# Performance work log

Measured on AMD Instinct MI355X. Metric: run time of the kernel, lower is better.

## Reference

```python
import jax, jax.numpy as jnp
import numpy as np

B, T, C, H = 8, 1024, 768, 12
M = 8  # extra rows in feats left as zeros (n = M + B*T)
N = M + B * T


def setup_inputs() -> dict:
    key = jax.random.key(0)
    k1, k2, k3, k4, k5 = jax.random.split(key, 5)
    feats = jax.random.normal(k1, (N, C), dtype=jnp.float32)
    amask = jax.random.randint(k2, (B, T), 0, 2).astype(bool)
    Wqkv = jax.random.normal(k3, (3 * C, C), dtype=jnp.float32) * 0.02
    Wp = jax.random.normal(k4, (C, C), dtype=jnp.float32) * 0.02
    bp = jax.random.normal(k5, (C,), dtype=jnp.float32) * 0.001
    return {"feats": feats, "amask": amask, "Wqkv": Wqkv, "Wp": Wp, "bp": bp}


def reference(feats, amask, Wqkv, Wp, bp):
    b, t = amask.shape
    n, c = feats.shape
    m = n - b * t          # rows of feats not touched by attention (stay zero)
    h = H
    d = c // h
    scale = d ** -0.5
    mf = amask.reshape(-1)                      # [b*t] bool
    x = feats[m:]                               # [b*t, c]

    # MaskedLinear(qkv): gather->GEMM->scatter == dense GEMM zeroed at masked-out rows
    qkv = jnp.where(mf[:, None], x @ Wqkv.T, jnp.zeros((), x.dtype))  # [b*t, 3c]
    qkv = qkv.reshape(b, t, 3, h, d).transpose(2, 0, 3, 1, 4)          # [3,b,h,t,d]
    q, k, v = qkv[0], qkv[1], qkv[2]

    # dense SDPA (no attn mask, matching F.scaled_dot_product_attention default)
    att = jax.nn.softmax(jnp.einsum('bhqd,bhkd->bhqk', q, k) * scale, axis=-1)
    o = jnp.einsum('bhqk,bhkd->bhqd', att, v)                          # [b,h,t,d]
    o = o.transpose(0, 2, 1, 3).reshape(b * t, c)                      # [b*t, c]

    # MaskedLinear(proj) with bias; masked-out rows are zero (not bias)
    o = jnp.where(mf[:, None], o @ Wp.T + bp, jnp.zeros((), o.dtype))

    # scatter back into a zero tensor of feats' shape (first m rows zero)
    return jnp.concatenate([jnp.zeros((m, c), feats.dtype), o], axis=0)
```

## Files before the change

### kernel.cpp

```cpp
#include <hip/hip_runtime.h>
#include <hip/hip_bf16.h>


#define BB 8
#define TT 1024
#define CC 768
#define HH 12
#define DD 64
#define MM 8
#define NTOK (BB*TT)
#define NX (NTOK*CC)
#define NWQ (3*CC*CC)
#define NWP (CC*CC)
#define QSCALE 0.18033688011112042f

typedef short bf16x8 __attribute__((ext_vector_type(8)));
typedef float f32x4  __attribute__((ext_vector_type(4)));
typedef float f32x16 __attribute__((ext_vector_type(16)));

__device__ __forceinline__ void gld16(const void* g, void* l) {
  __builtin_amdgcn_global_load_lds(
      (const __attribute__((address_space(1))) void*)g,
      (__attribute__((address_space(3))) void*)l, 16, 0, 0);
}

__device__ __forceinline__ short bf_rne(float f) {
  unsigned u = __float_as_uint(f);
  return (short)((u + 0x7FFFu + ((u >> 16) & 1u)) >> 16);
}
__device__ __forceinline__ short bf_split(float f, short& lo) {
  unsigned u = __float_as_uint(f);
  unsigned hb = (u + 0x7FFFu + ((u >> 16) & 1u)) >> 16;
  float r = f - __uint_as_float(hb << 16);
  lo = bf_rne(r);
  return (short)hb;
}

__global__ __launch_bounds__(256) void split_inputs(
    const float* __restrict__ x, const float* __restrict__ wq,
    const float* __restrict__ wp,
    short* __restrict__ xh, short* __restrict__ wqh,
    short* __restrict__ wph, short* __restrict__ wpl,
    float* __restrict__ out) {
  const int G0 = NX/4, G1 = G0 + NWQ/4, G2 = G1 + NWP/4;
  int i = blockIdx.x * 256 + threadIdx.x;
  if (i < MM*CC/4) {
    float4 z = {0.f, 0.f, 0.f, 0.f};
    ((float4*)out)[i] = z;
  }
  if (i >= G2) return;
  if (i < G1) {
    const float* src = (i < G0) ? x : wq;
    short* dh = (i < G0) ? xh : wqh;
    int li = (i < G0) ? i : i - G0;
    float4 v = *(const float4*)(src + (size_t)li * 4);
    short4 h;
    h.x = bf_rne(v.x); h.y = bf_rne(v.y); h.z = bf_rne(v.z); h.w = bf_rne(v.w);
    *(short4*)(dh + (size_t)li * 4) = h;
  } else {
    int li = i - G1;
    float4 v = *(const float4*)(wp + (size_t)li * 4);
    short4 h, l;
    h.x = bf_split(v.x, l.x);
    h.y = bf_split(v.y, l.y);
    h.z = bf_split(v.z, l.z);
    h.w = bf_split(v.w, l.w);
    *(short4*)(wph + (size_t)li * 4) = h;
    *(short4*)(wpl + (size_t)li * 4) = l;
  }
}

template<bool TRIPLE>
__device__ __forceinline__ void gemm_core_768(
    const short* __restrict__ ah_g, const short* __restrict__ al_g,
    const short* __restrict__ bh_g, const short* __restrict__ bl_g,
    short* Ah, short* Al, short* Bh, short* Bl,
    int m0, int n0, f32x16 (&acc)[2][2],
    int& wm_o, int& wn_o) {
  const int tid = threadIdx.x;
  const int w = tid >> 6, ln = tid & 63;
  const int wm = (w >> 1) * 64, wn = (w & 1) * 64;
  const int sr = ln >> 2;
  const int sc = (((ln & 3) ^ ((ln >> 3) & 3))) * 8;
  const int l31 = ln & 31, lhi = ln >> 5;
  const int key = (l31 >> 1) & 3;
  const int c0 = 2*w, c1 = 2*w + 1;
  const short* gAh0 = ah_g + (size_t)(m0 + c0*16 + sr)*CC + sc;
  const short* gAh1 = ah_g + (size_t)(m0 + c1*16 + sr)*CC + sc;
  const short* gBh0 = bh_g + (size_t)(n0 + c0*16 + sr)*CC + sc;
  const short* gBh1 = bh_g + (size_t)(n0 + c1*16 + sr)*CC + sc;
  const short* gAl0 = TRIPLE ? al_g + (size_t)(m0 + c0*16 + sr)*CC + sc : nullptr;
  const short* gAl1 = TRIPLE ? al_g + (size_t)(m0 + c1*16 + sr)*CC + sc : nullptr;
  const short* gBl0 = TRIPLE ? bl_g + (size_t)(n0 + c0*16 + sr)*CC + sc : nullptr;
  const short* gBl1 = TRIPLE ? bl_g + (size_t)(n0 + c1*16 + sr)*CC + sc : nullptr;
  #pragma unroll
  for (int i = 0; i < 2; i++)
    #pragma unroll
    for (int j = 0; j < 2; j++)
      #pragma unroll
      for (int r = 0; r < 16; r++) acc[i][j][r] = 0.f;

  for (int it = 0; it < 24; ++it) {
    const int ko = it * 32;
    gld16(gAh0 + ko, &Ah[c0*512]);
    gld16(gAh1 + ko, &Ah[c1*512]);
    gld16(gBh0 + ko, &Bh[c0*512]);
    gld16(gBh1 + ko, &Bh[c1*512]);
    if constexpr (TRIPLE) {
      gld16(gAl0 + ko, &Al[c0*512]);
      gld16(gAl1 + ko, &Al[c1*512]);
      gld16(gBl0 + ko, &Bl[c0*512]);
      gld16(gBl1 + ko, &Bl[c1*512]);
    }
    __syncthreads();
    bf16x8 a_h[2][2], b_h[2][2];
    #pragma unroll
    for (int t = 0; t < 2; ++t)
      #pragma unroll
      for (int kc = 0; kc < 2; ++kc) {
        const int sA = ((kc*2 + lhi) ^ key) * 8;
        a_h[t][kc] = *(const bf16x8*)&Ah[(wm + t*32 + l31)*32 + sA];
        b_h[t][kc] = *(const bf16x8*)&Bh[(wn + t*32 + l31)*32 + sA];
      }
    if constexpr (TRIPLE) {
      bf16x8 a_l[2][2], b_l[2][2];
      #pragma unroll
      for (int t = 0; t < 2; ++t)
        #pragma unroll
        for (int kc = 0; kc < 2; ++kc) {
          const int sA = ((kc*2 + lhi) ^ key) * 8;
          a_l[t][kc] = *(const bf16x8*)&Al[(wm + t*32 + l31)*32 + sA];
          b_l[t][kc] = *(const bf16x8*)&Bl[(wn + t*32 + l31)*32 + sA];
        }
      #pragma unroll
      for (int mt = 0; mt < 2; ++mt)
        #pragma unroll
        for (int nt = 0; nt < 2; ++nt)
          #pragma unroll
          for (int kc = 0; kc < 2; ++kc) {
            acc[mt][nt] = __builtin_amdgcn_mfma_f32_32x32x16_bf16(
                a_h[mt][kc], b_h[nt][kc], acc[mt][nt], 0, 0, 0);
            acc[mt][nt] = __builtin_amdgcn_mfma_f32_32x32x16_bf16(
                a_h[mt][kc], b_l[nt][kc], acc[mt][nt], 0, 0, 0);
            acc[mt][nt] = __builtin_amdgcn_mfma_f32_32x32x16_bf16(
                a_l[mt][kc], b_h[nt][kc], acc[mt][nt], 0, 0, 0);
          }
    } else {
      #pragma unroll
      for (int mt = 0; mt < 2; ++mt)
        #pragma unroll
        for (int nt = 0; nt < 2; ++nt)
          #pragma unroll
          for (int kc = 0; kc < 2; ++kc)
            acc[mt][nt] = __builtin_amdgcn_mfma_f32_32x32x16_bf16(
                a_h[mt][kc], b_h[nt][kc], acc[mt][nt], 0, 0, 0);
    }
    __syncthreads();
  }
  wm_o = wm; wn_o = wn;
}

__global__ __launch_bounds__(256) void qkv_mfma(
    const short* __restrict__ xh, const short* __restrict__ wqh,
    const int* __restrict__ mask,
    short* __restrict__ qb, short* __restrict__ kb, short* __restrict__ vbt) {
  __shared__ __align__(16) short Ah[128*32], Bh[128*32];
  const int m0 = blockIdx.x * 128, n0 = blockIdx.y * 128;
  const int s = n0 / CC;
  f32x16 acc[2][2];
  int wm, wn;
  const int ln = threadIdx.x & 63;
  const int l31 = ln & 31, lhi = ln >> 5;

  if (s < 2) {
    gemm_core_768<false>(xh, nullptr, wqh, nullptr,
                         Ah, nullptr, Bh, nullptr, m0, n0, acc, wm, wn);
    short* dst = (s == 0) ? qb : kb;
    const float qs = (s == 0) ? QSCALE : 1.f;
    const int nb = n0 % CC;
    #pragma unroll
    for (int mt = 0; mt < 2; ++mt) {
      #pragma unroll
      for (int reg = 0; reg < 16; ++reg) {
        int row = m0 + wm + mt*32 + 4*lhi + (reg & 3) + 8*(reg >> 2);
        int mk = mask[row];
        int b = row >> 10, t = row & 1023;
        size_t rb = ((size_t)b * HH) * TT;
        #pragma unroll
        for (int nt = 0; nt < 2; ++nt) {
          int gnb = nb + wn + nt*32 + l31;
          int h = gnb >> 6, d = gnb & 63;
          float v = mk ? acc[mt][nt][reg] * qs : 0.f;
          dst[((rb + (size_t)h * TT) + t) * DD + d] = bf_rne(v);
        }
      }
    }
  } else {
    gemm_core_768<false>(wqh, nullptr, xh, nullptr,
                         Ah, nullptr, Bh, nullptr, n0, m0, acc, wm, wn);
    const int b = m0 >> 10, t0 = m0 & 1023;
    #pragma unroll
    for (int mt = 0; mt < 2; ++mt) {
      #pragma unroll
      for (int reg = 0; reg < 16; ++reg) {
        int f = (n0 - 2*CC) + wm + mt*32 + 4*lhi + (reg & 3) + 8*(reg >> 2);
        int h = f >> 6, d = f & 63;
        short* drow = vbt + (((size_t)(b*HH + h)*DD) + d)*TT + t0;
        #pragma unroll
        for (int nt = 0; nt < 2; ++nt) {
          int tk = wn + nt*32 + l31;
          int mk = mask[m0 + tk];
          drow[tk] = bf_rne(mk ? acc[mt][nt][reg] : 0.f);
        }
      }
    }
  }
}

__global__ __launch_bounds__(256) void proj_mfma(
    const short* __restrict__ ah_g, const short* __restrict__ al_g,
    const short* __restrict__ bh_g, const short* __restrict__ bl_g,
    const int* __restrict__ mask, const float* __restrict__ bp,
    float* __restrict__ out) {
  __shared__ __align__(16) short Ah[128*32], Al[128*32];
  __shared__ __align__(16) short Bh[128*32], Bl[128*32];
  const int m0 = blockIdx.x * 128, n0 = blockIdx.y * 128;
  f32x16 acc[2][2];
  int wm, wn;
  gemm_core_768<true>(ah_g, al_g, bh_g, bl_g, Ah, Al, Bh, Bl, m0, n0, acc, wm, wn);
  const int ln = threadIdx.x & 63;
  const int l31 = ln & 31, lhi = ln >> 5;
  #pragma unroll
  for (int mt = 0; mt < 2; ++mt) {
    #pragma unroll
    for (int reg = 0; reg < 16; ++reg) {
      int row = m0 + wm + mt*32 + 4*lhi + (reg & 3) + 8*(reg >> 2);
      int mk = mask[row];
      float* orow = out + (size_t)(MM + row) * CC;
      #pragma unroll
      for (int nt = 0; nt < 2; ++nt) {
        int gn = n0 + wn + nt*32 + l31;
        orow[gn] = mk ? acc[mt][nt][reg] + bp[gn] : 0.f;
      }
    }
  }
}

__global__ __launch_bounds__(256) void attn_mfma(
    const short* __restrict__ qb, const short* __restrict__ kb,
    const short* __restrict__ vbt, const int* __restrict__ mask,
    short* __restrict__ obh, short* __restrict__ obl) {
  __shared__ __align__(16) short Ks[64][72];
  __shared__ __align__(16) short Vt[64][72];
  __shared__ __align__(16) short Ps[4][32][72];
  const int tid = threadIdx.x, w = tid >> 6, ln = tid & 63;
  const int fl = ln & 15, fq = ln >> 4;
  const int i = blockIdx.x;
  const int bh = i % 96;
  const int q0 = (i / 96) * 128;
  const int b = bh / HH, h = bh % HH;
  const size_t baseK = (size_t)bh * TT * DD;
  const size_t baseV = (size_t)bh * DD * TT;

  bf16x8 qf[2][2];
  #pragma unroll
  for (int mt = 0; mt < 2; ++mt)
    #pragma unroll
    for (int kc = 0; kc < 2; ++kc)
      qf[mt][kc] = *(const bf16x8*)&qb[baseK +
          (size_t)(q0 + w*32 + mt*16 + fl) * DD + kc*32 + fq*8];

  f32x4 oa[2][4];
  float lsum[2][4];
  {
    f32x4 z = {0.f, 0.f, 0.f, 0.f};
    #pragma unroll
    for (int mt = 0; mt < 2; ++mt) {
      #pragma unroll
      for (int nt = 0; nt < 4; ++nt) oa[mt][nt] = z;
      #pragma unroll
      for (int r = 0; r < 4; ++r) lsum[mt][r] = 0.f;
    }
  }

  const int srow = tid >> 2, scol = (tid & 3) * 16;
  const short* kg = &kb[baseK + (size_t)srow * DD + scol];
  const short* vg = &vbt[baseV + (size_t)srow * TT + scol];

  bf16x8 rk0 = *(const bf16x8*)kg;
  bf16x8 rk1 = *(const bf16x8*)(kg + 8);
  bf16x8 rv0 = *(const bf16x8*)vg;
  bf16x8 rv1 = *(const bf16x8*)(vg + 8);
  *(bf16x8*)&Ks[srow][scol]     = rk0;
  *(bf16x8*)&Ks[srow][scol + 8] = rk1;
  *(bf16x8*)&Vt[srow][scol]     = rv0;
  *(bf16x8*)&Vt[srow][scol + 8] = rv1;
  asm volatile("s_waitcnt lgkmcnt(0)" ::: "memory");
  __builtin_amdgcn_s_barrier();

  for (int kt = 0; kt < 16; ++kt) {
    if (kt < 15) {
      const short* kgn = kg + (size_t)(kt + 1) * 64 * DD;
      const short* vgn = vg + (kt + 1) * 64;
      rk0 = *(const bf16x8*)kgn;
      rk1 = *(const bf16x8*)(kgn + 8);
      rv0 = *(const bf16x8*)vgn;
      rv1 = *(const bf16x8*)(vgn + 8);
    }

    bf16x8 kf[4][2], vf[4][2];
    #pragma unroll
    for (int nt = 0; nt < 4; ++nt)
      #pragma unroll
      for (int kc = 0; kc < 2; ++kc) {
        kf[nt][kc] = *(const bf16x8*)&Ks[nt*16 + fl][kc*32 + fq*8];
        vf[nt][kc] = *(const bf16x8*)&Vt[nt*16 + fl][kc*32 + fq*8];
      }

    f32x4 s[2][4];
    {
      f32x4 z = {0.f, 0.f, 0.f, 0.f};
      #pragma unroll
      for (int mt = 0; mt < 2; ++mt)
        #pragma unroll
        for (int nt = 0; nt < 4; ++nt) s[mt][nt] = z;
    }
    #pragma unroll
    for (int mt = 0; mt < 2; ++mt)
      #pragma unroll
      for (int nt = 0; nt < 4; ++nt) {
        s[mt][nt] = __builtin_amdgcn_mfma_f32_16x16x32_bf16(
            qf[mt][0], kf[nt][0], s[mt][nt], 0, 0, 0);
        s[mt][nt] = __builtin_amdgcn_mfma_f32_16x16x32_bf16(
            qf[mt][1], kf[nt][1], s[mt][nt], 0, 0, 0);
      }

    #pragma unroll
    for (int mt = 0; mt < 2; ++mt)
      #pragma unroll
      for (int nt = 0; nt < 4; ++nt)
        #pragma unroll
        for (int r = 0; r < 4; ++r) {
          float p = __builtin_amdgcn_exp2f(s[mt][nt][r]);
          unsigned pu = __float_as_uint(p);
          lsum[mt][r] += __uint_as_float(pu & 0xFFFF0000u);
          Ps[w][mt*16 + fq*4 + r][nt*16 + fl] = (short)(pu >> 16);
        }

    bf16x8 pf[2][2];
    #pragma unroll
    for (int mt = 0; mt < 2; ++mt)
      #pragma unroll
      for (int kc = 0; kc < 2; ++kc)
        pf[mt][kc] = *(const bf16x8*)&Ps[w][mt*16 + fl][kc*32 + fq*8];

    #pragma unroll
    for (int mt = 0; mt < 2; ++mt)
      #pragma unroll
      for (int nt = 0; nt < 4; ++nt) {
        oa[mt][nt] = __builtin_amdgcn_mfma_f32_16x16x32_bf16(
            pf[mt][0], vf[nt][0], oa[mt][nt], 0, 0, 0);
        oa[mt][nt] = __builtin_amdgcn_mfma_f32_16x16x32_bf16(
            pf[mt][1], vf[nt][1], oa[mt][nt], 0, 0, 0);
      }

    __builtin_amdgcn_s_barrier();
    __builtin_amdgcn_sched_barrier(0);
    if (kt < 15) {
      *(bf16x8*)&Ks[srow][scol]     = rk0;
      *(bf16x8*)&Ks[srow][scol + 8] = rk1;
      *(bf16x8*)&Vt[srow][scol]     = rv0;
      *(bf16x8*)&Vt[srow][scol + 8] = rv1;
      asm volatile("s_waitcnt lgkmcnt(0)" ::: "memory");
    }
    __builtin_amdgcn_s_barrier();
  }

  #pragma unroll
  for (int mt = 0; mt < 2; ++mt)
    #pragma unroll
    for (int r = 0; r < 4; ++r) {
      float v = lsum[mt][r];
      v += __shfl_xor(v, 1);
      v += __shfl_xor(v, 2);
      v += __shfl_xor(v, 4);
      v += __shfl_xor(v, 8);
      lsum[mt][r] = v;
    }

  #pragma unroll
  for (int mt = 0; mt < 2; ++mt)
    #pragma unroll
    for (int r = 0; r < 4; ++r) {
      int tok = b * TT + q0 + w*32 + mt*16 + fq*4 + r;
      int mk = mask[tok];
      float inv = 1.f / lsum[mt][r];
      size_t ro = (size_t)tok * CC + h * DD;
      #pragma unroll
      for (int nt = 0; nt < 4; ++nt) {
        float v = mk ? oa[mt][nt][r] * inv : 0.f;
        short lo, hi = bf_split(v, lo);
        obh[ro + nt*16 + fl] = hi;
        obl[ro + nt*16 + fl] = lo;
      }
    }
}

extern "C" void kernel_launch(void* const* d_in, const int* in_sizes, int n_in,
                              void* d_out, int out_size, void* d_ws, size_t ws_size,
                              hipStream_t stream) {
  const float* feats = (const float*)d_in[0];
  const int*   mask  = (const int*)d_in[1];
  const float* Wqkv  = (const float*)d_in[2];
  const float* Wp    = (const float*)d_in[3];
  const float* bp    = (const float*)d_in[4];
  float* out = (float*)d_out;

  short* qb   = (short*)d_ws;
  short* kb   = qb + NX;
  short* vbt  = kb + NX;
  short* S_hi = vbt + NX;
  short* S_lo = S_hi + NX;
  short* wqh  = S_lo + NX;
  short* wph  = wqh + NWQ;
  short* wpl  = wph + NWP;

  const int G2 = (NX + NWQ + NWP) / 4;
  split_inputs<<<dim3((G2 + 255)/256), dim3(256), 0, stream>>>(
      feats + (size_t)MM * CC, Wqkv, Wp, S_hi, wqh, wph, wpl, out);
  qkv_mfma<<<dim3(NTOK/128, 3*CC/128), dim3(256), 0, stream>>>(
      S_hi, wqh, mask, qb, kb, vbt);
  attn_mfma<<<dim3(BB*HH*(TT/128)), dim3(256), 0, stream>>>(
      qb, kb, vbt, mask, S_hi, S_lo);
  proj_mfma<<<dim3(NTOK/128, CC/128), dim3(256), 0, stream>>>(
      S_hi, S_lo, wph, wpl, mask, bp, out);
}
```

Before: 221.0 us.

## Shrink attention query tile to 64 rows per block and raise occupancy

The attention kernel now has each wave handle 16 query rows instead of 32, so a block covers 64 queries and the grid doubles to 1536 blocks. Register arrays and the per-wave P scratch in LDS shrink, V fragment loads move after the softmax step, and launch bounds request 5 blocks per CU. The goal is better occupancy and latency hiding on the 256-CU part. The cost is that each K/V tile is loaded from global memory and staged through LDS twice as often per query, which halves K/V reuse.

```diff
diff --git a/kernel.cpp b/kernel.cpp
--- a/kernel.cpp
+++ b/kernel.cpp
@@ -246,41 +246,36 @@
   }
 }
 
-__global__ __launch_bounds__(256) void attn_mfma(
+__global__ __launch_bounds__(256, 5) void attn_mfma(
     const short* __restrict__ qb, const short* __restrict__ kb,
     const short* __restrict__ vbt, const int* __restrict__ mask,
     short* __restrict__ obh, short* __restrict__ obl) {
   __shared__ __align__(16) short Ks[64][72];
   __shared__ __align__(16) short Vt[64][72];
-  __shared__ __align__(16) short Ps[4][32][72];
+  __shared__ __align__(16) short Ps[4][16][72];
   const int tid = threadIdx.x, w = tid >> 6, ln = tid & 63;
   const int fl = ln & 15, fq = ln >> 4;
   const int i = blockIdx.x;
   const int bh = i % 96;
-  const int q0 = (i / 96) * 128;
+  const int q0 = (i / 96) * 64;
   const int b = bh / HH, h = bh % HH;
   const size_t baseK = (size_t)bh * TT * DD;
   const size_t baseV = (size_t)bh * DD * TT;
 
-  bf16x8 qf[2][2];
+  bf16x8 qf[2];
   #pragma unroll
-  for (int mt = 0; mt < 2; ++mt)
-    #pragma unroll
-    for (int kc = 0; kc < 2; ++kc)
-      qf[mt][kc] = *(const bf16x8*)&qb[baseK +
-          (size_t)(q0 + w*32 + mt*16 + fl) * DD + kc*32 + fq*8];
-
-  f32x4 oa[2][4];
-  float lsum[2][4];
+  for (int kc = 0; kc < 2; ++kc)
+    qf[kc] = *(const bf16x8*)&qb[baseK +
+        (size_t)(q0 + w*16 + fl) * DD + kc*32 + fq*8];
+
+  f32x4 oa[4];
+  float lsum[4];
   {
     f32x4 z = {0.f, 0.f, 0.f, 0.f};
     #pragma unroll
-    for (int mt = 0; mt < 2; ++mt) {
-      #pragma unroll
-      for (int nt = 0; nt < 4; ++nt) oa[mt][nt] = z;
-      #pragma unroll
-      for (int r = 0; r < 4; ++r) lsum[mt][r] = 0.f;
-    }
+    for (int nt = 0; nt < 4; ++nt) oa[nt] = z;
+    #pragma unroll
+    for (int r = 0; r < 4; ++r) lsum[r] = 0.f;
   }
 
   const int srow = tid >> 2, scol = (tid & 3) * 16;
@@ -308,61 +303,56 @@
       rv1 = *(const bf16x8*)(vgn + 8);
     }
 
-    bf16x8 kf[4][2], vf[4][2];
+    bf16x8 kf[4][2];
     #pragma unroll
     for (int nt = 0; nt < 4; ++nt)
       #pragma unroll
-      for (int kc = 0; kc < 2; ++kc) {
+      for (int kc = 0; kc < 2; ++kc)
         kf[nt][kc] = *(const bf16x8*)&Ks[nt*16 + fl][kc*32 + fq*8];
-        vf[nt][kc] = *(const bf16x8*)&Vt[nt*16 + fl][kc*32 + fq*8];
-      }
-
-    f32x4 s[2][4];
+
+    f32x4 s[4];
     {
       f32x4 z = {0.f, 0.f, 0.f, 0.f};
       #pragma unroll
-      for (int mt = 0; mt < 2; ++mt)
-        #pragma unroll
-        for (int nt = 0; nt < 4; ++nt) s[mt][nt] = z;
-    }
-    #pragma unroll
-    for (int mt = 0; mt < 2; ++mt)
-      #pragma unroll
-      for (int nt = 0; nt < 4; ++nt) {
-        s[mt][nt] = __builtin_amdgcn_mfma_f32_16x16x32_bf16(
-            qf[mt][0], kf[nt][0], s[mt][nt], 0, 0, 0);
-        s[mt][nt] = __builtin_amdgcn_mfma_f32_16x16x32_bf16(
-            qf[mt][1], kf[nt][1], s[mt][nt], 0, 0, 0);
+      for (int nt = 0; nt < 4; ++nt) s[nt] = z;
+    }
+    #pragma unroll
+    for (int nt = 0; nt < 4; ++nt) {
+      s[nt] = __builtin_amdgcn_mfma_f32_16x16x32_bf16(
+          qf[0], kf[nt][0], s[nt], 0, 0, 0);
+      s[nt] = __builtin_amdgcn_mfma_f32_16x16x32_bf16(
+          qf[1], kf[nt][1], s[nt], 0, 0, 0);
+    }
+
+    #pragma unroll
+    for (int nt = 0; nt < 4; ++nt)
+      #pragma unroll
+      for (int r = 0; r < 4; ++r) {
+        float p = __builtin_amdgcn_exp2f(s[nt][r]);
+        unsigned pu = __float_as_uint(p);
+        lsum[r] += __uint_as_float(pu & 0xFFFF0000u);
+        Ps[w][fq*4 + r][nt*16 + fl] = (short)(pu >> 16);
       }
 
-    #pragma unroll
-    for (int mt = 0; mt < 2; ++mt)
-      #pragma unroll
-      for (int nt = 0; nt < 4; ++nt)
-        #pragma unroll
-        for (int r = 0; r < 4; ++r) {
-          float p = __builtin_amdgcn_exp2f(s[mt][nt][r]);
-          unsigned pu = __float_as_uint(p);
-          lsum[mt][r] += __uint_as_float(pu & 0xFFFF0000u);
-          Ps[w][mt*16 + fq*4 + r][nt*16 + fl] = (short)(pu >> 16);
-        }
-
-    bf16x8 pf[2][2];
-    #pragma unroll
-    for (int mt = 0; mt < 2; ++mt)
+    bf16x8 vf[4][2];
+    #pragma unroll
+    for (int nt = 0; nt < 4; ++nt)
       #pragma unroll
       for (int kc = 0; kc < 2; ++kc)
-        pf[mt][kc] = *(const bf16x8*)&Ps[w][mt*16 + fl][kc*32 + fq*8];
-
-    #pragma unroll
-    for (int mt = 0; mt < 2; ++mt)
-      #pragma unroll
-      for (int nt = 0; nt < 4; ++nt) {
-        oa[mt][nt] = __builtin_amdgcn_mfma_f32_16x16x32_bf16(
-            pf[mt][0], vf[nt][0], oa[mt][nt], 0, 0, 0);
-        oa[mt][nt] = __builtin_amdgcn_mfma_f32_16x16x32_bf16(
-            pf[mt][1], vf[nt][1], oa[mt][nt], 0, 0, 0);
-      }
+        vf[nt][kc] = *(const bf16x8*)&Vt[nt*16 + fl][kc*32 + fq*8];
+
+    bf16x8 pf[2];
+    #pragma unroll
+    for (int kc = 0; kc < 2; ++kc)
+      pf[kc] = *(const bf16x8*)&Ps[w][fl][kc*32 + fq*8];
+
+    #pragma unroll
+    for (int nt = 0; nt < 4; ++nt) {
+      oa[nt] = __builtin_amdgcn_mfma_f32_16x16x32_bf16(
+          pf[0], vf[nt][0], oa[nt], 0, 0, 0);
+      oa[nt] = __builtin_amdgcn_mfma_f32_16x16x32_bf16(
+          pf[1], vf[nt][1], oa[nt], 0, 0, 0);
+    }
 
     __builtin_amdgcn_s_barrier();
     __builtin_amdgcn_sched_barrier(0);
@@ -377,33 +367,29 @@
   }
 
   #pragma unroll
-  for (int mt = 0; mt < 2; ++mt)
-    #pragma unroll
-    for (int r = 0; r < 4; ++r) {
-      float v = lsum[mt][r];
-      v += __shfl_xor(v, 1);
-      v += __shfl_xor(v, 2);
-      v += __shfl_xor(v, 4);
-      v += __shfl_xor(v, 8);
-      lsum[mt][r] = v;
-    }
+  for (int r = 0; r < 4; ++r) {
+    float v = lsum[r];
+    v += __shfl_xor(v, 1);
+    v += __shfl_xor(v, 2);
+    v += __shfl_xor(v, 4);
+    v += __shfl_xor(v, 8);
+    lsum[r] = v;
+  }
 
   #pragma unroll
-  for (int mt = 0; mt < 2; ++mt)
-    #pragma unroll
-    for (int r = 0; r < 4; ++r) {
-      int tok = b * TT + q0 + w*32 + mt*16 + fq*4 + r;
-      int mk = mask[tok];
-      float inv = 1.f / lsum[mt][r];
-      size_t ro = (size_t)tok * CC + h * DD;
-      #pragma unroll
-      for (int nt = 0; nt < 4; ++nt) {
-        float v = mk ? oa[mt][nt][r] * inv : 0.f;
-        short lo, hi = bf_split(v, lo);
-        obh[ro + nt*16 + fl] = hi;
-        obl[ro + nt*16 + fl] = lo;
-      }
-    }
+  for (int r = 0; r < 4; ++r) {
+    int tok = b * TT + q0 + w*16 + fq*4 + r;
+    int mk = mask[tok];
+    float inv = 1.f / lsum[r];
+    size_t ro = (size_t)tok * CC + h * DD;
+    #pragma unroll
+    for (int nt = 0; nt < 4; ++nt) {
+      float v = mk ? oa[nt][r] * inv : 0.f;
+      short lo, hi = bf_split(v, lo);
+      obh[ro + nt*16 + fl] = hi;
+      obl[ro + nt*16 + fl] = lo;
+    }
+  }
 }
 
 extern "C" void kernel_launch(void* const* d_in, const int* in_sizes, int n_in,
@@ -430,7 +416,7 @@
       feats + (size_t)MM * CC, Wqkv, Wp, S_hi, wqh, wph, wpl, out);
   qkv_mfma<<<dim3(NTOK/128, 3*CC/128), dim3(256), 0, stream>>>(
       S_hi, wqh, mask, qb, kb, vbt);
-  attn_mfma<<<dim3(BB*HH*(TT/128)), dim3(256), 0, stream>>>(
+  attn_mfma<<<dim3(96 * (TT/64)), dim3(256), 0, stream>>>(
       qb, kb, vbt, mask, S_hi, S_lo);
   proj_mfma<<<dim3(NTOK/128, CC/128), dim3(256), 0, stream>>>(
       S_hi, S_lo, wph, wpl, mask, bp, out);
```

Result: no change. 220.4 us (-0.3%).

## Store P transposed and reload with ds_read_b64_tr_b16 in attention kernel

Applied to the files above, without the earlier changes.

The P tile is now written to LDS as packed 64-bit words in a transposed layout, replacing the 16-bit scattered stores. It is read back with the gfx950 ds_read_b64_tr_b16 transpose-load instruction, which cuts the number of LDS store instructions and bank conflicts. V fragment loads move after the QK MFMAs to reduce register pressure, and launch_bounds adds a minimum of 3 blocks per CU for occupancy. The explicit waitcnts and the sched_barrier limit how much the compiler can overlap work.

```diff
diff --git a/kernel.cpp b/kernel.cpp
--- a/kernel.cpp
+++ b/kernel.cpp
@@ -14,9 +14,11 @@
 #define NWP (CC*CC)
 #define QSCALE 0.18033688011112042f
 
+typedef short bf16x4 __attribute__((ext_vector_type(4)));
 typedef short bf16x8 __attribute__((ext_vector_type(8)));
 typedef float f32x4  __attribute__((ext_vector_type(4)));
 typedef float f32x16 __attribute__((ext_vector_type(16)));
+typedef unsigned int u32x2 __attribute__((ext_vector_type(2)));
 
 __device__ __forceinline__ void gld16(const void* g, void* l) {
   __builtin_amdgcn_global_load_lds(
@@ -246,13 +248,20 @@
   }
 }
 
-__global__ __launch_bounds__(256) void attn_mfma(
+__device__ __forceinline__ bf16x4 tr64(unsigned addr, int imm) {
+  bf16x4 r;
+  asm volatile("ds_read_b64_tr_b16 %0, %1 offset:%c2"
+               : "=v"(r) : "v"(addr), "i"(imm));
+  return r;
+}
+
+__global__ __launch_bounds__(256, 3) void attn_mfma(
     const short* __restrict__ qb, const short* __restrict__ kb,
     const short* __restrict__ vbt, const int* __restrict__ mask,
     short* __restrict__ obh, short* __restrict__ obl) {
   __shared__ __align__(16) short Ks[64][72];
   __shared__ __align__(16) short Vt[64][72];
-  __shared__ __align__(16) short Ps[4][32][72];
+  __shared__ __align__(16) short PsT[4][2][64][16];
   const int tid = threadIdx.x, w = tid >> 6, ln = tid & 63;
   const int fl = ln & 15, fq = ln >> 4;
   const int i = blockIdx.x;
@@ -282,6 +291,9 @@
       for (int r = 0; r < 4; ++r) lsum[mt][r] = 0.f;
     }
   }
+
+  const unsigned ps_rd =
+      (unsigned)(size_t)(&PsT[0][0][0][0]) + w*4096 + fq*256 + fl*8;
 
   const int srow = tid >> 2, scol = (tid & 3) * 16;
   const short* kg = &kb[baseK + (size_t)srow * DD + scol];
@@ -308,14 +320,12 @@
       rv1 = *(const bf16x8*)(vgn + 8);
     }
 
-    bf16x8 kf[4][2], vf[4][2];
+    bf16x8 kf[4][2];
     #pragma unroll
     for (int nt = 0; nt < 4; ++nt)
       #pragma unroll
-      for (int kc = 0; kc < 2; ++kc) {
+      for (int kc = 0; kc < 2; ++kc)
         kf[nt][kc] = *(const bf16x8*)&Ks[nt*16 + fl][kc*32 + fq*8];
-        vf[nt][kc] = *(const bf16x8*)&Vt[nt*16 + fl][kc*32 + fq*8];
-      }
 
     f32x4 s[2][4];
     {
@@ -335,24 +345,44 @@
             qf[mt][1], kf[nt][1], s[mt][nt], 0, 0, 0);
       }
 
+    bf16x8 vf[4][2];
+    #pragma unroll
+    for (int nt = 0; nt < 4; ++nt)
+      #pragma unroll
+      for (int kc = 0; kc < 2; ++kc)
+        vf[nt][kc] = *(const bf16x8*)&Vt[nt*16 + fl][kc*32 + fq*8];
+
     #pragma unroll
     for (int mt = 0; mt < 2; ++mt)
       #pragma unroll
-      for (int nt = 0; nt < 4; ++nt)
-        #pragma unroll
-        for (int r = 0; r < 4; ++r) {
-          float p = __builtin_amdgcn_exp2f(s[mt][nt][r]);
-          unsigned pu = __float_as_uint(p);
-          lsum[mt][r] += __uint_as_float(pu & 0xFFFF0000u);
-          Ps[w][mt*16 + fq*4 + r][nt*16 + fl] = (short)(pu >> 16);
-        }
+      for (int nt = 0; nt < 4; ++nt) {
+        unsigned u0 = __float_as_uint(__builtin_amdgcn_exp2f(s[mt][nt][0]));
+        unsigned u1 = __float_as_uint(__builtin_amdgcn_exp2f(s[mt][nt][1]));
+        unsigned u2 = __float_as_uint(__builtin_amdgcn_exp2f(s[mt][nt][2]));
+        unsigned u3 = __float_as_uint(__builtin_amdgcn_exp2f(s[mt][nt][3]));
+        lsum[mt][0] += __uint_as_float(u0 & 0xFFFF0000u);
+        lsum[mt][1] += __uint_as_float(u1 & 0xFFFF0000u);
+        lsum[mt][2] += __uint_as_float(u2 & 0xFFFF0000u);
+        lsum[mt][3] += __uint_as_float(u3 & 0xFFFF0000u);
+        u32x2 pw;
+        pw[0] = (u0 >> 16) | (u1 & 0xFFFF0000u);
+        pw[1] = (u2 >> 16) | (u3 & 0xFFFF0000u);
+        *(u32x2*)&PsT[w][mt][nt*16 + fl][fq*4] = pw;
+      }
+
+    asm volatile("s_waitcnt lgkmcnt(0)" ::: "memory");
 
     bf16x8 pf[2][2];
     #pragma unroll
     for (int mt = 0; mt < 2; ++mt)
       #pragma unroll
-      for (int kc = 0; kc < 2; ++kc)
-        pf[mt][kc] = *(const bf16x8*)&Ps[w][mt*16 + fl][kc*32 + fq*8];
+      for (int kc = 0; kc < 2; ++kc) {
+        bf16x4 lo = tr64(ps_rd, mt*2048 + kc*1024);
+        bf16x4 hi = tr64(ps_rd, mt*2048 + kc*1024 + 128);
+        pf[mt][kc] = __builtin_shufflevector(lo, hi, 0, 1, 2, 3, 4, 5, 6, 7);
+      }
+    asm volatile("s_waitcnt lgkmcnt(0)" ::: "memory");
+    __builtin_amdgcn_sched_barrier(0);
 
     #pragma unroll
     for (int mt = 0; mt < 2; ++mt)
@@ -430,7 +460,7 @@
       feats + (size_t)MM * CC, Wqkv, Wp, S_hi, wqh, wph, wpl, out);
   qkv_mfma<<<dim3(NTOK/128, 3*CC/128), dim3(256), 0, stream>>>(
       S_hi, wqh, mask, qb, kb, vbt);
-  attn_mfma<<<dim3(BB*HH*(TT/128)), dim3(256), 0, stream>>>(
+  attn_mfma<<<dim3(96 * (TT/128)), dim3(256), 0, stream>>>(
       qb, kb, vbt, mask, S_hi, S_lo);
   proj_mfma<<<dim3(NTOK/128, CC/128), dim3(256), 0, stream>>>(
       S_hi, S_lo, wph, wpl, mask, bp, out);
```

Measured after the change: 213.4 us. -3.5%, faster.
